# Kernel tuning notes

Measured on AMD Instinct MI355X. Metric: run time of the kernel, lower is better.

The kernel has to match this reference:

```python
import jax, jax.numpy as jnp
import numpy as np

DIM = 1536
NUM_HEADS = 16
HEAD_DIM = DIM // NUM_HEADS  # 96
ROPE_DIM = HEAD_DIM // 2     # 48
PT_SEQ = 32
FT_SEQ = 32
EPS = 1e-6


def _rope_tables():
    # VisionRotaryEmbedding(dim=48, pt_seq_len=32): 2D axial rotary tables
    f = 1.0 / (10000.0 ** (np.arange(0, ROPE_DIM, 2, dtype=np.float32)[: ROPE_DIM // 2] / ROPE_DIM))
    pos = np.arange(FT_SEQ, dtype=np.float32) / FT_SEQ * PT_SEQ
    freqs = pos[:, None] * f[None, :]                       # [32, 24]
    freqs = np.repeat(freqs, 2, axis=-1)                    # [32, 48] interleaved
    row = np.broadcast_to(freqs[:, None, :], (FT_SEQ, FT_SEQ, ROPE_DIM))
    col = np.broadcast_to(freqs[None, :, :], (FT_SEQ, FT_SEQ, ROPE_DIM))
    grid = np.concatenate([row, col], axis=-1).reshape(-1, HEAD_DIM)  # [1024, 96]
    return jnp.asarray(np.cos(grid)), jnp.asarray(np.sin(grid))


def _apply_rotary(x, cos, sin):
    # x: [B, S, H, D]; cos/sin: [S, D]; interleaved (use_real_unbind_dim=-1) rotation
    xr = x.reshape(*x.shape[:-1], -1, 2)
    x_rot = jnp.stack([-xr[..., 1], xr[..., 0]], axis=-1).reshape(x.shape)
    return x * cos[None, :, None, :] + x_rot * sin[None, :, None, :]


def _rms_norm(x, w):
    var = jnp.mean(jnp.square(x), axis=-1, keepdims=True)
    return x * jax.lax.rsqrt(var + EPS) * w


def setup_inputs() -> dict:
    key = jax.random.key(0)
    ks = jax.random.split(key, 12)
    s = 1.0 / np.sqrt(DIM)
    return {
        "hidden_states": jax.random.normal(ks[0], (8, 1024, DIM), dtype=jnp.float32),
        "Wq": jax.random.normal(ks[1], (DIM, DIM), dtype=jnp.float32) * s,
        "bq": jax.random.normal(ks[2], (DIM,), dtype=jnp.float32) * 0.01,
        "Wk": jax.random.normal(ks[3], (DIM, DIM), dtype=jnp.float32) * s,
        "bk": jax.random.normal(ks[4], (DIM,), dtype=jnp.float32) * 0.01,
        "Wv": jax.random.normal(ks[5], (DIM, DIM), dtype=jnp.float32) * s,
        "bv": jax.random.normal(ks[6], (DIM,), dtype=jnp.float32) * 0.01,
        "q_norm_w": jnp.ones((HEAD_DIM,), dtype=jnp.float32),
        "k_norm_w": jnp.ones((HEAD_DIM,), dtype=jnp.float32),
        "Wo": jax.random.normal(ks[7], (DIM, DIM), dtype=jnp.float32) * s,
        "bo": jax.random.normal(ks[8], (DIM,), dtype=jnp.float32) * 0.01,
    }


def reference(hidden_states, Wq, bq, Wk, bk, Wv, bv, q_norm_w, k_norm_w, Wo, bo):
    B, S, _ = hidden_states.shape
    cos, sin = _rope_tables()  # [S, HEAD_DIM], constants

    q = hidden_states @ Wq.T + bq
    k = hidden_states @ Wk.T + bk
    v = hidden_states @ Wv.T + bv
    q = q.reshape(B, S, NUM_HEADS, HEAD_DIM)
    k = k.reshape(B, S, NUM_HEADS, HEAD_DIM)
    v = v.reshape(B, S, NUM_HEADS, HEAD_DIM)

    q = _rms_norm(q, q_norm_w)
    k = _rms_norm(k, k_norm_w)
    q = _apply_rotary(q, cos, sin)
    k = _apply_rotary(k, cos, sin)

    scale = 1.0 / np.sqrt(HEAD_DIM)
    scores = jnp.einsum("bshd,bthd->bhst", q, k) * scale  # [B, H, S, S]
    probs = jax.nn.softmax(scores, axis=-1)
    out = jnp.einsum("bhst,bthd->bshd", probs, v)          # [B, S, H, D]
    out = out.reshape(B, S, DIM)
    return out @ Wo.T + bo
```

## Files before the change

### kernel.cpp

```cpp
#include <hip/hip_runtime.h>
#include <hip/hip_bf16.h>
#include <math.h>

typedef __hip_bfloat16 bf16;
typedef __attribute__((ext_vector_type(8))) short short8;
typedef __attribute__((ext_vector_type(4))) short short4v;
typedef __attribute__((ext_vector_type(4))) float f32x4;

#define MFMA16(a, b, c) __builtin_amdgcn_mfma_f32_16x16x32_bf16((a), (b), (c), 0, 0, 0)

typedef const __attribute__((address_space(1))) void GVOID;
typedef __attribute__((address_space(3))) void LVOID;

__device__ __forceinline__ float b2f(short s) {
    union { unsigned u; float f; } v;
    v.u = ((unsigned)(unsigned short)s) << 16;
    return v.f;
}
__device__ __forceinline__ short f2b(float f) {
    union { float f; unsigned u; } v;
    v.f = f;
    unsigned r = v.u + 0x7fffu + ((v.u >> 16) & 1u);
    return (short)(r >> 16);
}
__device__ __forceinline__ unsigned packbf(float a, float b) {
    return ((unsigned)(unsigned short)f2b(a)) | (((unsigned)(unsigned short)f2b(b)) << 16);
}

__global__ void sniff_kernel(const unsigned* __restrict__ X, int* __restrict__ flag) {
    __shared__ int cnt;
    if (threadIdx.x == 0) cnt = 0;
    __syncthreads();
    int c = 0;
    for (int i = threadIdx.x; i < 256; i += 64) {
        unsigned w = X[i];
        unsigned e = (w >> 7) & 0xFFu;
        c += (e > 140u) ? 1 : 0;
    }
    atomicAdd(&cnt, c);
    __syncthreads();
    if (threadIdx.x == 0) *flag = (cnt >= 16) ? 1 : 0;
}

__device__ __forceinline__ void canon8(const void* src, short* dst, int i, int f) {
    short8 o;
    if (f) {
        const float* s = (const float*)src + (size_t)i * 8;
#pragma unroll
        for (int j = 0; j < 8; ++j) o[j] = f2b(s[j]);
    } else {
        o = ((const short8*)src)[i];
    }
    ((short8*)dst)[i] = o;
}

__global__ __launch_bounds__(256) void canon_x_kernel(
    const void* __restrict__ src, short* __restrict__ dst, int n8,
    const int* __restrict__ flag)
{
    int i = blockIdx.x * 256 + threadIdx.x;
    if (i >= n8) return;
    canon8(src, dst, i, *flag);
}

__global__ __launch_bounds__(256) void canon_w4_kernel(
    const void* __restrict__ s0, const void* __restrict__ s1,
    const void* __restrict__ s2, const void* __restrict__ s3,
    short* __restrict__ d0, short* __restrict__ d1,
    short* __restrict__ d2, short* __restrict__ d3,
    const int* __restrict__ flag)
{
    const int m = blockIdx.y;
    const void* src = (m == 0) ? s0 : (m == 1) ? s1 : (m == 2) ? s2 : s3;
    short* dst = (m == 0) ? d0 : (m == 1) ? d1 : (m == 2) ? d2 : d3;
    int i = blockIdx.x * 256 + threadIdx.x;
    canon8(src, dst, i, *flag);
}

__global__ void canon_vec_kernel(
    const void* __restrict__ bq, const void* __restrict__ bk,
    const void* __restrict__ bv, const void* __restrict__ bo,
    const void* __restrict__ qw, const void* __restrict__ kw,
    float* __restrict__ biasqkv, float* __restrict__ boc,
    float* __restrict__ qwc, float* __restrict__ kwc,
    const int* __restrict__ flag)
{
    const int f = *flag;
    for (int i = threadIdx.x; i < 6336; i += 256) {
        const void* src; float* dst; int j;
        if (i < 4608) {
            int m = i / 1536; j = i - m * 1536;
            src = (m == 0) ? bq : (m == 1) ? bk : bv; dst = biasqkv + i;
        } else if (i < 6144) { j = i - 4608; src = bo; dst = boc + j; }
        else if (i < 6240)   { j = i - 6144; src = qw; dst = qwc + j; }
        else                 { j = i - 6240; src = kw; dst = kwc + j; }
        *dst = f ? ((const float*)src)[j] : b2f(((const short*)src)[j]);
    }
}

__global__ void rope_tables_kernel(float* __restrict__ cosT, float* __restrict__ sinT) {
    int idx = blockIdx.x * 256 + threadIdx.x;
    if (idx >= 1024 * 96) return;
    int p = idx / 96;
    int d = idx - p * 96;
    int r = p >> 5, c = p & 31;
    int inRow = (d < 48);
    int dd = inRow ? d : d - 48;
    float pos = inRow ? (float)r : (float)c;
    float ex = -(float)(dd & ~1) / 48.0f;
    float f = powf(10000.0f, ex);
    float ang = pos * f;
    cosT[idx] = cosf(ang);
    sinT[idx] = sinf(ang);
}

__global__ __launch_bounds__(512) void gemm256_kernel(
    const bf16* __restrict__ A, const bf16* __restrict__ Bw,
    const float* __restrict__ bias,
    bf16* __restrict__ O0, bf16* __restrict__ O1, bf16* __restrict__ O2,
    int K, const int* __restrict__ outFlag)
{
    __shared__ __align__(16) short As[2][256 * 32];
    __shared__ __align__(16) short Bs[2][256 * 32];

    const int tid = threadIdx.x;
    const int lane = tid & 63, w = tid >> 6;
    const int wm = w >> 2, wn = w & 3;
    const int li = lane & 15, lg = lane >> 4;

    const int total = gridDim.x * gridDim.y;
    const int pp = blockIdx.y * gridDim.x + blockIdx.x;
    const int lb = (pp & 7) * (total >> 3) + (pp >> 3);
    const int nb = lb % gridDim.x;
    const int mb = lb / gridDim.x;
    const long mBase = (long)mb * 256;
    const long nGlob = (long)nb * 256;

    const bf16* aSrc[2]; const bf16* bSrc[2]; int ldsOff[2];
#pragma unroll
    for (int u = 0; u < 2; ++u) {
        const int L = u * 8192 + tid * 16;
        const int S = L ^ (((L >> 7) & 3) << 4);
        const int srow = S >> 6;
        const int scol = (S & 63) >> 1;
        aSrc[u] = A + (mBase + srow) * K + scol;
        bSrc[u] = Bw + (nGlob + srow) * K + scol;
        ldsOff[u] = L >> 1;
    }
    const int koff = ((lg * 16) ^ (((li >> 1) & 3) << 4)) >> 1;

    f32x4 acc[8][4] = {};
    const int NT = K >> 5;

    auto stage = [&](int tt, int bb) {
        const long kc = (long)tt * 32;
#pragma unroll
        for (int u = 0; u < 2; ++u)
            __builtin_amdgcn_global_load_lds((GVOID*)(aSrc[u] + kc),
                                             (LVOID*)&As[bb][ldsOff[u]], 16, 0, 0);
#pragma unroll
        for (int u = 0; u < 2; ++u)
            __builtin_amdgcn_global_load_lds((GVOID*)(bSrc[u] + kc),
                                             (LVOID*)&Bs[bb][ldsOff[u]], 16, 0, 0);
    };

    stage(0, 0);
    asm volatile("s_waitcnt vmcnt(0)" ::: "memory");
    __builtin_amdgcn_s_barrier();
    asm volatile("" ::: "memory");

    for (int t = 0; t < NT; ++t) {
        const int cb = t & 1;
        if (t + 1 < NT) stage(t + 1, cb ^ 1);
        const short* Ab = &As[cb][0];
        const short* Bb = &Bs[cb][0];
        short8 fb[4], fa[4];
#pragma unroll
        for (int n = 0; n < 4; ++n)
            fb[n] = *(const short8*)(Bb + (wn * 64 + n * 16 + li) * 32 + koff);
#pragma unroll
        for (int m = 0; m < 4; ++m)
            fa[m] = *(const short8*)(Ab + (wm * 128 + m * 16 + li) * 32 + koff);
        __builtin_amdgcn_sched_barrier(0);
        __builtin_amdgcn_s_setprio(1);
#pragma unroll
        for (int m = 0; m < 4; ++m)
#pragma unroll
            for (int n = 0; n < 4; ++n)
                acc[m][n] = MFMA16(fa[m], fb[n], acc[m][n]);
        __builtin_amdgcn_s_setprio(0);
        __builtin_amdgcn_sched_barrier(0);
#pragma unroll
        for (int m = 0; m < 4; ++m)
            fa[m] = *(const short8*)(Ab + (wm * 128 + 64 + m * 16 + li) * 32 + koff);
        __builtin_amdgcn_sched_barrier(0);
        __builtin_amdgcn_s_setprio(1);
#pragma unroll
        for (int m = 0; m < 4; ++m)
#pragma unroll
            for (int n = 0; n < 4; ++n)
                acc[4 + m][n] = MFMA16(fa[m], fb[n], acc[4 + m][n]);
        __builtin_amdgcn_s_setprio(0);
        __builtin_amdgcn_sched_barrier(0);
        asm volatile("s_waitcnt vmcnt(0)" ::: "memory");
        __builtin_amdgcn_s_barrier();
        asm volatile("" ::: "memory");
    }

    const int f32out = outFlag ? *outFlag : 0;
    const int mat = nb / 6;
    const long colBase = nGlob - (long)mat * 1536;
    bf16* Ob = (mat == 0) ? O0 : (mat == 1) ? O1 : O2;
    if (f32out) {
        float* Cf = (float*)Ob;
#pragma unroll
        for (int n = 0; n < 4; ++n) {
            const long col = colBase + wn * 64 + n * 16 + li;
            const float bv = bias[nGlob + wn * 64 + n * 16 + li];
#pragma unroll
            for (int m = 0; m < 8; ++m) {
                const long row = mBase + wm * 128 + m * 16 + lg * 4;
#pragma unroll
                for (int i = 0; i < 4; ++i)
                    Cf[(row + i) * 1536 + col] = acc[m][n][i] + bv;
            }
        }
    } else {
#pragma unroll
        for (int n = 0; n < 4; ++n) {
            const long col = colBase + wn * 64 + n * 16 + li;
            const float bv = bias[nGlob + wn * 64 + n * 16 + li];
#pragma unroll
            for (int m = 0; m < 8; ++m) {
                const long row = mBase + wm * 128 + m * 16 + lg * 4;
#pragma unroll
                for (int i = 0; i < 4; ++i)
                    Ob[(row + i) * 1536 + col] = __float2bfloat16(acc[m][n][i] + bv);
            }
        }
    }
}

__global__ __launch_bounds__(256) void norm_rope_kernel(
    bf16* __restrict__ T, const float* __restrict__ wgt,
    const float* __restrict__ cosT, const float* __restrict__ sinT,
    float scale)
{
    const int row = blockIdx.x * 256 + threadIdx.x;
    const int tok = row >> 4;
    const int h = row & 15;
    const int spos = tok & 1023;
    bf16* p = T + (size_t)tok * 1536 + h * 96;

    float x[96];
#pragma unroll
    for (int v = 0; v < 12; ++v) {
        short8 t = *(const short8*)(p + v * 8);
#pragma unroll
        for (int j = 0; j < 8; ++j) x[v * 8 + j] = b2f(t[j]);
    }
    float ss = 0.f;
#pragma unroll
    for (int d = 0; d < 96; ++d) ss += x[d] * x[d];
    const float rn = scale / sqrtf(ss * (1.0f / 96.0f) + 1e-6f);

    const float* cr = cosT + spos * 96;
    const float* sr = sinT + spos * 96;

#pragma unroll
    for (int v = 0; v < 12; ++v) {
        short8 o;
#pragma unroll
        for (int j = 0; j < 8; j += 2) {
            const int d = v * 8 + j;
            const float x0 = x[d] * rn * wgt[d];
            const float x1 = x[d + 1] * rn * wgt[d + 1];
            o[j]     = f2b(x0 * cr[d] - x1 * sr[d]);
            o[j + 1] = f2b(x1 * cr[d + 1] + x0 * sr[d + 1]);
        }
        *(short8*)(p + v * 8) = o;
    }
}

__global__ __launch_bounds__(256) void attn_kernel(
    const bf16* __restrict__ Q, const bf16* __restrict__ K,
    const bf16* __restrict__ V, bf16* __restrict__ O)
{
    __shared__ __align__(16) short Ks[64 * 100];
    __shared__ __align__(16) short Vt[96 * 76];
    __shared__ __align__(16) short Pl[4][32 * 72];

    const int tid = threadIdx.x;
    const int l = tid & 63, w = tid >> 6;
    const int li = l & 15, lg = l >> 4;

    const int p = blockIdx.x;
    const int lb = (p & 7) * 128 + (p >> 3);
    const int qt = lb & 7;
    const int bh = lb >> 3;
    const int b = bh >> 4, h = bh & 15;
    const size_t tokBase = (size_t)b * 1024;

    short8 aq[2][3];
#pragma unroll
    for (int r = 0; r < 2; ++r) {
        const bf16* qp = Q + (tokBase + qt * 128 + w * 32 + r * 16 + li) * 1536 + h * 96;
#pragma unroll
        for (int kk = 0; kk < 3; ++kk)
            aq[r][kk] = *(const short8*)(qp + kk * 32 + lg * 8);
    }

    float m_r[2] = {-1e30f, -1e30f};
    float l_r[2] = {0.f, 0.f};
    f32x4 o[2][6] = {};

    int kr[3], km[3];
#pragma unroll
    for (int u = 0; u < 3; ++u) {
        const int c = tid + 256 * u;
        kr[u] = c / 12;
        km[u] = (c - kr[u] * 12) * 8;
    }
    const int vr = tid >> 2;
    const int vc0 = (tid & 3) * 24;
    short* Plw = &Pl[w][0];

    short8 kreg[3], vreg[3];
#pragma unroll
    for (int u = 0; u < 3; ++u)
        kreg[u] = *(const short8*)(K + (tokBase + kr[u]) * 1536 + h * 96 + km[u]);
    {
        const bf16* vp = V + (tokBase + vr) * 1536 + h * 96 + vc0;
#pragma unroll
        for (int u = 0; u < 3; ++u) vreg[u] = *(const short8*)(vp + u * 8);
    }

    for (int t0 = 0; t0 < 1024; t0 += 64) {
        __syncthreads();
#pragma unroll
        for (int u = 0; u < 3; ++u)
            *(short8*)&Ks[kr[u] * 100 + km[u]] = kreg[u];
#pragma unroll
        for (int u = 0; u < 3; ++u)
#pragma unroll
            for (int j = 0; j < 8; ++j)
                Vt[(vc0 + u * 8 + j) * 76 + vr] = vreg[u][j];
        __syncthreads();

        const int t1 = (t0 + 64 < 1024) ? t0 + 64 : t0;
#pragma unroll
        for (int u = 0; u < 3; ++u)
            kreg[u] = *(const short8*)(K + (tokBase + t1 + kr[u]) * 1536 + h * 96 + km[u]);
        {
            const bf16* vp = V + (tokBase + t1 + vr) * 1536 + h * 96 + vc0;
#pragma unroll
            for (int u = 0; u < 3; ++u) vreg[u] = *(const short8*)(vp + u * 8);
        }

        f32x4 s4[2][4] = {};
#pragma unroll
        for (int kk = 0; kk < 3; ++kk) {
            short8 fk[4];
#pragma unroll
            for (int kn = 0; kn < 4; ++kn)
                fk[kn] = *(const short8*)&Ks[(kn * 16 + li) * 100 + kk * 32 + lg * 8];
#pragma unroll
            for (int r = 0; r < 2; ++r)
#pragma unroll
                for (int kn = 0; kn < 4; ++kn)
                    s4[r][kn] = MFMA16(fk[kn], aq[r][kk], s4[r][kn]);
        }

#pragma unroll
        for (int r = 0; r < 2; ++r) {
            float mk[4];
#pragma unroll
            for (int kn = 0; kn < 4; ++kn)
                mk[kn] = fmaxf(fmaxf(s4[r][kn][0], s4[r][kn][1]),
                               fmaxf(s4[r][kn][2], s4[r][kn][3]));
            float pm = fmaxf(fmaxf(mk[0], mk[1]), fmaxf(mk[2], mk[3]));
            pm = fmaxf(pm, __shfl_xor(pm, 16));
            pm = fmaxf(pm, __shfl_xor(pm, 32));

            float alpha = 1.0f;
            const bool need = (pm > m_r[r] + 8.0f);
            if (need) { alpha = exp2f(m_r[r] - pm); m_r[r] = pm; }
            const float mn = m_r[r];

            float rs = 0.f;
            unsigned pw[8];
#pragma unroll
            for (int kn = 0; kn < 4; ++kn) {
                float p0 = exp2f(s4[r][kn][0] - mn);
                float p1 = exp2f(s4[r][kn][1] - mn);
                float p2 = exp2f(s4[r][kn][2] - mn);
                float p3 = exp2f(s4[r][kn][3] - mn);
                rs += (p0 + p1) + (p2 + p3);
                pw[kn * 2]     = packbf(p0, p1);
                pw[kn * 2 + 1] = packbf(p2, p3);
            }
            rs += __shfl_xor(rs, 16);
            rs += __shfl_xor(rs, 32);
            l_r[r] = l_r[r] * alpha + rs;
            if (need) {
#pragma unroll
                for (int dn = 0; dn < 6; ++dn)
#pragma unroll
                    for (int i = 0; i < 4; ++i) o[r][dn][i] *= alpha;
            }
            unsigned* Pw = (unsigned*)Plw;
            const int rowW = ((r * 16 + li) * 72) >> 1;
#pragma unroll
            for (int kn = 0; kn < 4; ++kn) {
#pragma unroll
                for (int ip = 0; ip < 2; ++ip)
                    Pw[rowW + ((kn * 16 + lg * 4 + ip * 2) >> 1)] = pw[kn * 2 + ip];
            }
        }

#pragma unroll
        for (int kt = 0; kt < 2; ++kt) {
            short8 pa[2];
#pragma unroll
            for (int r = 0; r < 2; ++r)
                pa[r] = *(const short8*)&Plw[(r * 16 + li) * 72 + kt * 32 + lg * 8];
#pragma unroll
            for (int dn = 0; dn < 6; ++dn) {
                short8 fv = *(const short8*)&Vt[(dn * 16 + li) * 76 + kt * 32 + lg * 8];
#pragma unroll
                for (int r = 0; r < 2; ++r)
                    o[r][dn] = MFMA16(fv, pa[r], o[r][dn]);
            }
        }
    }

#pragma unroll
    for (int r = 0; r < 2; ++r) {
        const float inv = 1.0f / l_r[r];
        const size_t row = tokBase + qt * 128 + w * 32 + r * 16 + li;
#pragma unroll
        for (int dn = 0; dn < 6; ++dn) {
            short4v ov;
#pragma unroll
            for (int i = 0; i < 4; ++i) ov[i] = f2b(o[r][dn][i] * inv);
            *(short4v*)&O[row * 1536 + h * 96 + dn * 16 + lg * 4] = ov;
        }
    }
}

extern "C" void kernel_launch(void* const* d_in, const int* in_sizes, int n_in,
                              void* d_out, int out_size, void* d_ws, size_t ws_size,
                              hipStream_t stream) {
    const void* X  = d_in[0];
    const void* Wq = d_in[1];
    const void* bq = d_in[2];
    const void* Wk = d_in[3];
    const void* bk = d_in[4];
    const void* Wv = d_in[5];
    const void* bv = d_in[6];
    const void* qw = d_in[7];
    const void* kw = d_in[8];
    const void* Wo = d_in[9];
    const void* bo = d_in[10];

    char* ws = (char*)d_ws;
    size_t off = 0;
    int* flag = (int*)ws;                      off += 256;
    float* cosT = (float*)(ws + off);          off += 1024 * 96 * 4;
    float* sinT = (float*)(ws + off);          off += 1024 * 96 * 4;
    float* biasqkv = (float*)(ws + off);       off += 4608 * 4;
    float* boc  = (float*)(ws + off);          off += 1536 * 4;
    float* qwc  = (float*)(ws + off);          off += 128 * 4;
    float* kwc  = (float*)(ws + off);          off += 128 * 4;
    off = (off + 255) & ~(size_t)255;
    bf16* Wc  = (bf16*)(ws + off);             off += (size_t)4608 * 1536 * 2;
    bf16* Woc = (bf16*)(ws + off);             off += (size_t)1536 * 1536 * 2;
    bf16* Xc  = (bf16*)(ws + off);             off += (size_t)8192 * 1536 * 2;
    bf16* Qb  = (bf16*)(ws + off);             off += (size_t)8192 * 1536 * 2;
    bf16* Kb  = (bf16*)(ws + off);             off += (size_t)8192 * 1536 * 2;
    bf16* Vb  = (bf16*)(ws + off);             off += (size_t)8192 * 1536 * 2;
    bf16* AO  = Xc;

    sniff_kernel<<<1, 64, 0, stream>>>((const unsigned*)X, flag);

    canon_x_kernel<<<6144, 256, 0, stream>>>(X, (short*)Xc, 8192 * 1536 / 8, flag);
    canon_w4_kernel<<<dim3(1152, 4), 256, 0, stream>>>(
        Wq, Wk, Wv, Wo,
        (short*)Wc, (short*)(Wc + (size_t)1536 * 1536), (short*)(Wc + (size_t)2 * 1536 * 1536),
        (short*)Woc, flag);
    canon_vec_kernel<<<1, 256, 0, stream>>>(bq, bk, bv, bo, qw, kw,
                                            biasqkv, boc, qwc, kwc, flag);
    rope_tables_kernel<<<384, 256, 0, stream>>>(cosT, sinT);

    gemm256_kernel<<<dim3(18, 32), 512, 0, stream>>>(
        Xc, Wc, biasqkv, Qb, Kb, Vb, 1536, nullptr);

    const float qscale = (float)(0.10206207261596577 * 1.4426950408889634);
    norm_rope_kernel<<<512, 256, 0, stream>>>(Qb, qwc, cosT, sinT, qscale);
    norm_rope_kernel<<<512, 256, 0, stream>>>(Kb, kwc, cosT, sinT, 1.0f);

    attn_kernel<<<1024, 256, 0, stream>>>(Qb, Kb, Vb, AO);

    gemm256_kernel<<<dim3(6, 32), 512, 0, stream>>>(
        AO, Woc, boc, (bf16*)d_out, (bf16*)d_out, (bf16*)d_out, 1536, flag);
}
```

Measured before the change: 461.5 us.

## Switch GEMM to 128x128x64 tiles and repack V transpose in attention

```diff
diff --git a/kernel.cpp b/kernel.cpp
--- a/kernel.cpp
+++ b/kernel.cpp
@@ -23,8 +23,16 @@
     unsigned r = v.u + 0x7fffu + ((v.u >> 16) & 1u);
     return (short)(r >> 16);
 }
-__device__ __forceinline__ unsigned packbf(float a, float b) {
-    return ((unsigned)(unsigned short)f2b(a)) | (((unsigned)(unsigned short)f2b(b)) << 16);
+__device__ __forceinline__ unsigned packbf2(float a, float b) {
+    float2 t; t.x = a; t.y = b;
+    __hip_bfloat162 h = __float22bfloat162_rn(t);
+    union { __hip_bfloat162 h; unsigned u; } cv; cv.h = h;
+    return cv.u;
+}
+__device__ __forceinline__ short bf2s(float x) {
+    __hip_bfloat16 h = __float2bfloat16(x);
+    union { __hip_bfloat16 h; short s; } cv; cv.h = h;
+    return cv.s;
 }
 
 __global__ void sniff_kernel(const unsigned* __restrict__ X, int* __restrict__ flag) {
@@ -114,18 +122,18 @@
     sinT[idx] = sinf(ang);
 }
 
-__global__ __launch_bounds__(512) void gemm256_kernel(
+__global__ __launch_bounds__(256) void gemm128_kernel(
     const bf16* __restrict__ A, const bf16* __restrict__ Bw,
     const float* __restrict__ bias,
     bf16* __restrict__ O0, bf16* __restrict__ O1, bf16* __restrict__ O2,
     int K, const int* __restrict__ outFlag)
 {
-    __shared__ __align__(16) short As[2][256 * 32];
-    __shared__ __align__(16) short Bs[2][256 * 32];
+    __shared__ __align__(16) short As[2][128 * 64];
+    __shared__ __align__(16) short Bs[2][128 * 64];
 
     const int tid = threadIdx.x;
     const int lane = tid & 63, w = tid >> 6;
-    const int wm = w >> 2, wn = w & 3;
+    const int wr = w >> 1, wc = w & 1;
     const int li = lane & 15, lg = lane >> 4;
 
     const int total = gridDim.x * gridDim.y;
@@ -133,33 +141,37 @@
     const int lb = (pp & 7) * (total >> 3) + (pp >> 3);
     const int nb = lb % gridDim.x;
     const int mb = lb / gridDim.x;
-    const long mBase = (long)mb * 256;
-    const long nGlob = (long)nb * 256;
-
-    const bf16* aSrc[2]; const bf16* bSrc[2]; int ldsOff[2];
-#pragma unroll
-    for (int u = 0; u < 2; ++u) {
-        const int L = u * 8192 + tid * 16;
-        const int S = L ^ (((L >> 7) & 3) << 4);
-        const int srow = S >> 6;
-        const int scol = (S & 63) >> 1;
+    const long mBase = (long)mb * 128;
+    const long nGlob = (long)nb * 128;
+
+    const bf16* aSrc[4]; const bf16* bSrc[4]; int ldsOff[4];
+#pragma unroll
+    for (int u = 0; u < 4; ++u) {
+        const int L = u * 4096 + tid * 16;
+        const int S = L ^ (((L >> 7) & 7) << 4);
+        const int srow = S >> 7;
+        const int scol = (S & 127) >> 1;
         aSrc[u] = A + (mBase + srow) * K + scol;
         bSrc[u] = Bw + (nGlob + srow) * K + scol;
         ldsOff[u] = L >> 1;
     }
-    const int koff = ((lg * 16) ^ (((li >> 1) & 3) << 4)) >> 1;
-
-    f32x4 acc[8][4] = {};
-    const int NT = K >> 5;
+    const int rxor = (li & 7) << 4;
+    int kidx[2];
+#pragma unroll
+    for (int ks = 0; ks < 2; ++ks)
+        kidx[ks] = ((ks * 64 + lg * 16) ^ rxor) >> 1;
+
+    f32x4 acc[4][4] = {};
+    const int NT = K >> 6;
 
     auto stage = [&](int tt, int bb) {
-        const long kc = (long)tt * 32;
-#pragma unroll
-        for (int u = 0; u < 2; ++u)
+        const long kc = (long)tt * 64;
+#pragma unroll
+        for (int u = 0; u < 4; ++u)
             __builtin_amdgcn_global_load_lds((GVOID*)(aSrc[u] + kc),
                                              (LVOID*)&As[bb][ldsOff[u]], 16, 0, 0);
 #pragma unroll
-        for (int u = 0; u < 2; ++u)
+        for (int u = 0; u < 4; ++u)
             __builtin_amdgcn_global_load_lds((GVOID*)(bSrc[u] + kc),
                                              (LVOID*)&Bs[bb][ldsOff[u]], 16, 0, 0);
     };
@@ -174,52 +186,43 @@
         if (t + 1 < NT) stage(t + 1, cb ^ 1);
         const short* Ab = &As[cb][0];
         const short* Bb = &Bs[cb][0];
-        short8 fb[4], fa[4];
-#pragma unroll
-        for (int n = 0; n < 4; ++n)
-            fb[n] = *(const short8*)(Bb + (wn * 64 + n * 16 + li) * 32 + koff);
-#pragma unroll
-        for (int m = 0; m < 4; ++m)
-            fa[m] = *(const short8*)(Ab + (wm * 128 + m * 16 + li) * 32 + koff);
-        __builtin_amdgcn_sched_barrier(0);
-        __builtin_amdgcn_s_setprio(1);
-#pragma unroll
-        for (int m = 0; m < 4; ++m)
+#pragma unroll
+        for (int ks = 0; ks < 2; ++ks) {
+            short8 fa[4], fb[4];
+#pragma unroll
+            for (int m = 0; m < 4; ++m)
+                fa[m] = *(const short8*)(Ab + (wr * 64 + m * 16 + li) * 64 + kidx[ks]);
 #pragma unroll
             for (int n = 0; n < 4; ++n)
-                acc[m][n] = MFMA16(fa[m], fb[n], acc[m][n]);
-        __builtin_amdgcn_s_setprio(0);
-        __builtin_amdgcn_sched_barrier(0);
-#pragma unroll
-        for (int m = 0; m < 4; ++m)
-            fa[m] = *(const short8*)(Ab + (wm * 128 + 64 + m * 16 + li) * 32 + koff);
-        __builtin_amdgcn_sched_barrier(0);
-        __builtin_amdgcn_s_setprio(1);
-#pragma unroll
-        for (int m = 0; m < 4; ++m)
-#pragma unroll
-            for (int n = 0; n < 4; ++n)
-                acc[4 + m][n] = MFMA16(fa[m], fb[n], acc[4 + m][n]);
-        __builtin_amdgcn_s_setprio(0);
-        __builtin_amdgcn_sched_barrier(0);
+                fb[n] = *(const short8*)(Bb + (wc * 64 + n * 16 + li) * 64 + kidx[ks]);
+            __builtin_amdgcn_sched_barrier(0);
+            __builtin_amdgcn_s_setprio(1);
+#pragma unroll
+            for (int m = 0; m < 4; ++m)
+#pragma unroll
+                for (int n = 0; n < 4; ++n)
+                    acc[m][n] = MFMA16(fa[m], fb[n], acc[m][n]);
+            __builtin_amdgcn_s_setprio(0);
+            __builtin_amdgcn_sched_barrier(0);
+        }
         asm volatile("s_waitcnt vmcnt(0)" ::: "memory");
         __builtin_amdgcn_s_barrier();
         asm volatile("" ::: "memory");
     }
 
     const int f32out = outFlag ? *outFlag : 0;
-    const int mat = nb / 6;
+    const int mat = nb / 12;
     const long colBase = nGlob - (long)mat * 1536;
     bf16* Ob = (mat == 0) ? O0 : (mat == 1) ? O1 : O2;
     if (f32out) {
         float* Cf = (float*)Ob;
 #pragma unroll
         for (int n = 0; n < 4; ++n) {
-            const long col = colBase + wn * 64 + n * 16 + li;
-            const float bv = bias[nGlob + wn * 64 + n * 16 + li];
-#pragma unroll
-            for (int m = 0; m < 8; ++m) {
-                const long row = mBase + wm * 128 + m * 16 + lg * 4;
+            const long col = colBase + wc * 64 + n * 16 + li;
+            const float bv = bias[nGlob + wc * 64 + n * 16 + li];
+#pragma unroll
+            for (int m = 0; m < 4; ++m) {
+                const long row = mBase + wr * 64 + m * 16 + lg * 4;
 #pragma unroll
                 for (int i = 0; i < 4; ++i)
                     Cf[(row + i) * 1536 + col] = acc[m][n][i] + bv;
@@ -228,11 +231,11 @@
     } else {
 #pragma unroll
         for (int n = 0; n < 4; ++n) {
-            const long col = colBase + wn * 64 + n * 16 + li;
-            const float bv = bias[nGlob + wn * 64 + n * 16 + li];
-#pragma unroll
-            for (int m = 0; m < 8; ++m) {
-                const long row = mBase + wm * 128 + m * 16 + lg * 4;
+            const long col = colBase + wc * 64 + n * 16 + li;
+            const float bv = bias[nGlob + wc * 64 + n * 16 + li];
+#pragma unroll
+            for (int m = 0; m < 4; ++m) {
+                const long row = mBase + wr * 64 + m * 16 + lg * 4;
 #pragma unroll
                 for (int i = 0; i < 4; ++i)
                     Ob[(row + i) * 1536 + col] = __float2bfloat16(acc[m][n][i] + bv);
@@ -286,7 +289,7 @@
     const bf16* __restrict__ Q, const bf16* __restrict__ K,
     const bf16* __restrict__ V, bf16* __restrict__ O)
 {
-    __shared__ __align__(16) short Ks[64 * 100];
+    __shared__ __align__(16) short Ks[64 * 104];
     __shared__ __align__(16) short Vt[96 * 76];
     __shared__ __align__(16) short Pl[4][32 * 72];
 
@@ -321,30 +324,39 @@
         kr[u] = c / 12;
         km[u] = (c - kr[u] * 12) * 8;
     }
-    const int vr = tid >> 2;
-    const int vc0 = (tid & 3) * 24;
+    const int t2 = tid >> 3;
+    const int dh = tid & 7;
+    const bf16* vbase = V + (tokBase + 2 * t2) * 1536 + h * 96 + dh * 12;
     short* Plw = &Pl[w][0];
 
-    short8 kreg[3], vreg[3];
+    short8 kreg[3];
+    short4v vr0[3], vr1[3];
 #pragma unroll
     for (int u = 0; u < 3; ++u)
         kreg[u] = *(const short8*)(K + (tokBase + kr[u]) * 1536 + h * 96 + km[u]);
-    {
-        const bf16* vp = V + (tokBase + vr) * 1536 + h * 96 + vc0;
-#pragma unroll
-        for (int u = 0; u < 3; ++u) vreg[u] = *(const short8*)(vp + u * 8);
+#pragma unroll
+    for (int u = 0; u < 3; ++u) {
+        vr0[u] = *(const short4v*)(vbase + u * 4);
+        vr1[u] = *(const short4v*)(vbase + 1536 + u * 4);
     }
 
     for (int t0 = 0; t0 < 1024; t0 += 64) {
         __syncthreads();
 #pragma unroll
         for (int u = 0; u < 3; ++u)
-            *(short8*)&Ks[kr[u] * 100 + km[u]] = kreg[u];
-#pragma unroll
-        for (int u = 0; u < 3; ++u)
-#pragma unroll
-            for (int j = 0; j < 8; ++j)
-                Vt[(vc0 + u * 8 + j) * 76 + vr] = vreg[u][j];
+            *(short8*)&Ks[kr[u] * 104 + km[u]] = kreg[u];
+        {
+            unsigned* Vt32 = (unsigned*)Vt;
+#pragma unroll
+            for (int u = 0; u < 3; ++u)
+#pragma unroll
+                for (int j = 0; j < 4; ++j) {
+                    const int d = dh * 12 + u * 4 + j;
+                    const unsigned pk = ((unsigned)(unsigned short)vr0[u][j]) |
+                                        (((unsigned)(unsigned short)vr1[u][j]) << 16);
+                    Vt32[d * 38 + t2] = pk;
+                }
+        }
         __syncthreads();
 
         const int t1 = (t0 + 64 < 1024) ? t0 + 64 : t0;
@@ -352,9 +364,12 @@
         for (int u = 0; u < 3; ++u)
             kreg[u] = *(const short8*)(K + (tokBase + t1 + kr[u]) * 1536 + h * 96 + km[u]);
         {
-            const bf16* vp = V + (tokBase + t1 + vr) * 1536 + h * 96 + vc0;
-#pragma unroll
-            for (int u = 0; u < 3; ++u) vreg[u] = *(const short8*)(vp + u * 8);
+            const bf16* vp = vbase + (size_t)t1 * 1536;
+#pragma unroll
+            for (int u = 0; u < 3; ++u) {
+                vr0[u] = *(const short4v*)(vp + u * 4);
+                vr1[u] = *(const short4v*)(vp + 1536 + u * 4);
+            }
         }
 
         f32x4 s4[2][4] = {};
@@ -363,7 +378,7 @@
             short8 fk[4];
 #pragma unroll
             for (int kn = 0; kn < 4; ++kn)
-                fk[kn] = *(const short8*)&Ks[(kn * 16 + li) * 100 + kk * 32 + lg * 8];
+                fk[kn] = *(const short8*)&Ks[(kn * 16 + li) * 104 + kk * 32 + lg * 8];
 #pragma unroll
             for (int r = 0; r < 2; ++r)
 #pragma unroll
@@ -396,8 +411,8 @@
                 float p2 = exp2f(s4[r][kn][2] - mn);
                 float p3 = exp2f(s4[r][kn][3] - mn);
                 rs += (p0 + p1) + (p2 + p3);
-                pw[kn * 2]     = packbf(p0, p1);
-                pw[kn * 2 + 1] = packbf(p2, p3);
+                pw[kn * 2]     = packbf2(p0, p1);
+                pw[kn * 2 + 1] = packbf2(p2, p3);
             }
             rs += __shfl_xor(rs, 16);
             rs += __shfl_xor(rs, 32);
@@ -442,7 +457,7 @@
         for (int dn = 0; dn < 6; ++dn) {
             short4v ov;
 #pragma unroll
-            for (int i = 0; i < 4; ++i) ov[i] = f2b(o[r][dn][i] * inv);
+            for (int i = 0; i < 4; ++i) ov[i] = bf2s(o[r][dn][i] * inv);
             *(short4v*)&O[row * 1536 + h * 96 + dn * 16 + lg * 4] = ov;
         }
     }
@@ -492,7 +507,7 @@
                                             biasqkv, boc, qwc, kwc, flag);
     rope_tables_kernel<<<384, 256, 0, stream>>>(cosT, sinT);
 
-    gemm256_kernel<<<dim3(18, 32), 512, 0, stream>>>(
+    gemm128_kernel<<<dim3(36, 64), 256, 0, stream>>>(
         Xc, Wc, biasqkv, Qb, Kb, Vb, 1536, nullptr);
 
     const float qscale = (float)(0.10206207261596577 * 1.4426950408889634);
@@ -501,6 +516,6 @@
 
     attn_kernel<<<1024, 256, 0, stream>>>(Qb, Kb, Vb, AO);
 
-    gemm256_kernel<<<dim3(6, 32), 512, 0, stream>>>(
+    gemm128_kernel<<<dim3(12, 64), 256, 0, stream>>>(
         AO, Woc, boc, (bf16*)d_out, (bf16*)d_out, (bf16*)d_out, 1536, flag);
 }
```

Measured after the change: 384.7 us. -16.6%, faster.
